# Optimization experiments

Measured on AMD Instinct MI355X. Metric: run time of the kernel, lower is better.

## Reference

```python
import jax, jax.numpy as jnp
import numpy as np

HEADS = 16
D_K = 64  # hidden_size // heads = 1024 // 16
SCALE = D_K ** 0.5


def setup_inputs() -> dict:
    key = jax.random.key(0)
    ks = jax.random.split(key, 7)
    B, S, D = 4, 2048, 1024
    H = 1024  # hidden_size
    O = 1024  # outputs_dims
    s = 0.02
    return {
        "query": jax.random.normal(ks[0], (B, S, D), dtype=jnp.float32),
        "key": jax.random.normal(ks[1], (B, S, D), dtype=jnp.float32),
        "value": jax.random.normal(ks[2], (B, S, D), dtype=jnp.float32),
        "Wq": jax.random.normal(ks[3], (D, H), dtype=jnp.float32) * s,
        "Wk": jax.random.normal(ks[4], (D, H), dtype=jnp.float32) * s,
        "Wv": jax.random.normal(ks[5], (D, H), dtype=jnp.float32) * s,
        "Wo": jax.random.normal(ks[6], (H, O), dtype=jnp.float32) * s,
    }


def reference(query, key, value, Wq, Wk, Wv, Wo):
    B, S, _ = query.shape
    # Dense projections with relu activation (as in the original module)
    q = jax.nn.relu(query @ Wq).reshape(B, S, HEADS, D_K)  # [B,S,H,dk]
    k = jax.nn.relu(key @ Wk).reshape(B, S, HEADS, D_K)
    v = jax.nn.relu(value @ Wv).reshape(B, S, HEADS, D_K)
    # scores: [B,H,Sq,Sk]
    scores = jnp.einsum('bqhd,bkhd->bhqk', q, k) / SCALE
    attn = jax.nn.softmax(scores, axis=-1)
    # attention-weighted values -> [B,Sq,H,dk] -> [B,Sq,H*dk]
    ctx = jnp.einsum('bhqk,bkhd->bqhd', attn, v).reshape(B, S, HEADS * D_K)
    out = jax.nn.relu(ctx @ Wo)
    return out
```

## Files before the change

### kernel.cpp

```cpp
#include <hip/hip_runtime.h>

typedef unsigned short u16;
typedef __bf16 bf16x8 __attribute__((ext_vector_type(8)));
typedef float f32x4 __attribute__((ext_vector_type(4)));
typedef u16 u16x8 __attribute__((ext_vector_type(8)));
typedef u16 u16x4 __attribute__((ext_vector_type(4)));

#define MFMA16(a, b, c) __builtin_amdgcn_mfma_f32_16x16x32_bf16(a, b, c, 0, 0, 0)

static constexpr float QSC = 0.18033688011112042f;

__device__ inline u16 f2bf(float f) {
  union { float f; unsigned u; } x; x.f = f;
  unsigned r = x.u + 0x7FFF + ((x.u >> 16) & 1);
  return (u16)(r >> 16);
}
__device__ inline u16 cvt_bf(float f) {
  __bf16 h = (__bf16)f; return __builtin_bit_cast(u16, h);
}
__device__ inline bf16x8 ld_frag(const u16* p) {
  return __builtin_bit_cast(bf16x8, *(const u16x8*)p);
}
__device__ inline void dma16(const u16* g, u16* l) {
  __builtin_amdgcn_global_load_lds(
      (const __attribute__((address_space(1))) unsigned*)g,
      (__attribute__((address_space(3))) unsigned*)l, 16, 0, 0);
}

#if __has_builtin(__builtin_amdgcn_exp2f)
#define EXP2(x) __builtin_amdgcn_exp2f(x)
#else
#define EXP2(x) exp2f(x)
#endif

__launch_bounds__(256)
__global__ void prep_w(const float* __restrict__ Wq, const float* __restrict__ Wk,
                       const float* __restrict__ Wv, const float* __restrict__ Wo,
                       u16* __restrict__ Wt) {
  __shared__ u16 T[64 * 72];
  const int z = blockIdx.z;
  const float* W = z == 0 ? Wq : z == 1 ? Wk : z == 2 ? Wv : Wo;
  u16* D = Wt + ((size_t)z << 20);
  const int k0 = blockIdx.y * 64, c0 = blockIdx.x * 64;
  const int tid = threadIdx.x;
  const int kr = tid >> 2, cs = (tid & 3) * 16;
  const float* src = W + (size_t)(k0 + kr) * 1024 + c0 + cs;
  float f[16];
#pragma unroll
  for (int i = 0; i < 4; ++i) *(float4*)&f[i * 4] = ((const float4*)src)[i];
#pragma unroll
  for (int i = 0; i < 16; ++i) T[(cs + i) * 72 + kr] = cvt_bf(f[i]);
  __syncthreads();
  const int nn = tid >> 2, ks = (tid & 3) * 16;
  u16* dst = D + (size_t)(c0 + nn) * 1024 + k0 + ks;
  *(u16x8*)dst = *(u16x8*)&T[nn * 72 + ks];
  *(u16x8*)(dst + 8) = *(u16x8*)&T[nn * 72 + ks + 8];
}

__launch_bounds__(256)
__global__ void prep_a(const float* __restrict__ q, const float* __restrict__ k,
                       const float* __restrict__ v, u16* __restrict__ dq,
                       u16* __restrict__ dk, u16* __restrict__ dv) {
  const int z = blockIdx.z;
  const float* s = z == 0 ? q : z == 1 ? k : v;
  u16* d = z == 0 ? dq : z == 1 ? dk : dv;
  for (size_t i = blockIdx.x * 256 + threadIdx.x; i < (size_t)1048576; i += 262144) {
    const float* g = s + i * 8;
    float4 f0 = *(const float4*)g, f1 = *(const float4*)(g + 4);
    u16x8 h;
    h[0] = cvt_bf(f0.x); h[1] = cvt_bf(f0.y); h[2] = cvt_bf(f0.z); h[3] = cvt_bf(f0.w);
    h[4] = cvt_bf(f1.x); h[5] = cvt_bf(f1.y); h[6] = cvt_bf(f1.z); h[7] = cvt_bf(f1.w);
    *(u16x8*)(d + i * 8) = h;
  }
}

__launch_bounds__(512, 2)
__global__ void gemm_fwd(const u16* __restrict__ Aq, const u16* __restrict__ Ak,
                         const u16* __restrict__ Av, const u16* __restrict__ Wt,
                         u16* __restrict__ Qw, u16* __restrict__ Kw,
                         u16* __restrict__ Vw) {
  __shared__ u16 smem[49152];
  const int z = blockIdx.z;
  const u16* A = z == 0 ? Aq : z == 1 ? Ak : Av;
  const u16* Bt = Wt + ((size_t)z << 20);
  u16* out = z == 0 ? Qw : z == 1 ? Kw : Vw;
  const u16* Aop = (z == 2) ? Bt : A;
  const u16* Bop = (z == 2) ? A : Bt;

  const int tid = threadIdx.x;
  const int lane = tid & 63, l15 = lane & 15, quad = lane >> 4;
  const int wv = tid >> 6, wm = wv & 1, wn = wv >> 1;
  const int mblk = ((blockIdx.x & 7) << 2) | (blockIdx.x >> 3);
  const int m0 = (z == 2) ? blockIdx.y * 256 : mblk * 256;
  const int n0 = (z == 2) ? mblk * 256 : blockIdx.y * 256;

  const int cA0 = tid, cA1 = 512 + tid;
  const u16* gA0 = Aop + (size_t)(m0 + (cA0 & 255)) * 1024 + (cA0 >> 8) * 8;
  const u16* gA1 = Aop + (size_t)(m0 + (cA1 & 255)) * 1024 + (cA1 >> 8) * 8;
  const u16* gB0 = Bop + (size_t)(n0 + (cA0 & 255)) * 1024 + (cA0 >> 8) * 8;
  const u16* gB1 = Bop + (size_t)(n0 + (cA1 & 255)) * 1024 + (cA1 >> 8) * 8;
  const int ub0 = (wv * 64) * 8;
  const int ub1 = (512 + wv * 64) * 8;

  const int offA = (quad * 256 + wm * 128 + l15) * 8;
  const int offB = 8192 + (quad * 256 + wn * 64 + l15) * 8;

  f32x4 acc[8][4] = {};

  dma16(gA0, &smem[ub0]);
  dma16(gA1, &smem[ub1]);
  dma16(gB0, &smem[8192 + ub0]);
  dma16(gB1, &smem[8192 + ub1]);
  dma16(gA0 + 32, &smem[16384 + ub0]);
  dma16(gA1 + 32, &smem[16384 + ub1]);
  dma16(gB0 + 32, &smem[16384 + 8192 + ub0]);
  dma16(gB1 + 32, &smem[16384 + 8192 + ub1]);
  asm volatile("s_waitcnt vmcnt(4)" ::: "memory");
  __builtin_amdgcn_sched_barrier(0);
  __builtin_amdgcn_s_barrier();

  int bo0 = 0, bo1 = 16384, bo2 = 32768;
#pragma unroll 1
  for (int t = 0; t < 32; ++t) {
    if (t < 30) {
      dma16(gA0 + (t + 2) * 32, &smem[bo2 + ub0]);
      dma16(gA1 + (t + 2) * 32, &smem[bo2 + ub1]);
    }
    bf16x8 a[4], b[4];
#pragma unroll
    for (int j = 0; j < 4; ++j) b[j] = ld_frag(&smem[bo0 + offB + j * 128]);
#pragma unroll
    for (int i = 0; i < 4; ++i) a[i] = ld_frag(&smem[bo0 + offA + i * 128]);
    asm volatile("s_waitcnt lgkmcnt(0)" ::: "memory");
    __builtin_amdgcn_sched_barrier(0);
    __builtin_amdgcn_s_setprio(1);
#pragma unroll
    for (int i = 0; i < 4; ++i)
#pragma unroll
      for (int j = 0; j < 4; ++j)
        acc[i][j] = MFMA16(a[i], b[j], acc[i][j]);
    __builtin_amdgcn_s_setprio(0);
    __builtin_amdgcn_s_barrier();
    if (t < 30) {
      dma16(gB0 + (t + 2) * 32, &smem[bo2 + 8192 + ub0]);
      dma16(gB1 + (t + 2) * 32, &smem[bo2 + 8192 + ub1]);
    }
#pragma unroll
    for (int i = 0; i < 4; ++i) a[i] = ld_frag(&smem[bo0 + offA + (4 + i) * 128]);
    asm volatile("s_waitcnt lgkmcnt(0)" ::: "memory");
    __builtin_amdgcn_sched_barrier(0);
    __builtin_amdgcn_s_setprio(1);
#pragma unroll
    for (int i = 0; i < 4; ++i)
#pragma unroll
      for (int j = 0; j < 4; ++j)
        acc[4 + i][j] = MFMA16(a[i], b[j], acc[4 + i][j]);
    __builtin_amdgcn_s_setprio(0);
    if (t < 30) {
      asm volatile("s_waitcnt vmcnt(4)" ::: "memory");
      __builtin_amdgcn_sched_barrier(0);
    } else if (t == 30) {
      asm volatile("s_waitcnt vmcnt(0)" ::: "memory");
      __builtin_amdgcn_sched_barrier(0);
    }
    __builtin_amdgcn_s_barrier();
    const int tb = bo0; bo0 = bo1; bo1 = bo2; bo2 = tb;
  }

  if (z < 2) {
    const float sc = z == 0 ? QSC : 1.0f;
#pragma unroll
    for (int i = 0; i < 8; ++i)
#pragma unroll
      for (int j = 0; j < 4; ++j)
#pragma unroll
        for (int r = 0; r < 4; ++r) {
          float v = fmaxf(acc[i][j][r], 0.f) * sc;
          int m = m0 + wm * 128 + i * 16 + quad * 4 + r;
          int n = n0 + wn * 64 + j * 16 + l15;
          out[(size_t)m * 1024 + n] = f2bf(v);
        }
  } else {
    const int bb = n0 >> 11, s0 = n0 & 2047;
#pragma unroll
    for (int half = 0; half < 2; ++half) {
      __syncthreads();
      if ((wn >> 1) == half) {
#pragma unroll
        for (int i = 0; i < 8; ++i)
#pragma unroll
          for (int j = 0; j < 4; ++j)
#pragma unroll
            for (int r = 0; r < 4; ++r) {
              const int row = wm * 128 + i * 16 + quad * 4 + r;
              const int col = (wn & 1) * 64 + j * 16 + l15;
              smem[row * 128 + col] = f2bf(fmaxf(acc[i][j][r], 0.f));
            }
      }
      __syncthreads();
#pragma unroll
      for (int i2 = 0; i2 < 8; ++i2) {
        const int c = i2 * 512 + tid;
        const int row = c >> 4, ch = c & 15;
        u16* dst = out + (size_t)(bb * 1024 + m0 + row) * 2048 + s0 +
                   half * 128 + ch * 8;
        *(u16x8*)dst = *(u16x8*)&smem[row * 128 + ch * 8];
      }
    }
  }
}

__launch_bounds__(256, 3)
__global__ void gemm_out(const u16* __restrict__ A, const u16* __restrict__ Bt,
                         float* __restrict__ out) {
  __shared__ u16 smem[24576];
  const int tid = threadIdx.x;
  const int lane = tid & 63, l15 = lane & 15, quad = lane >> 4;
  const int wv = tid >> 6, wm = wv & 1, wn = wv >> 1;
  const int m0 = (blockIdx.x * 8 + (blockIdx.y >> 3)) * 128;
  const int n0 = (blockIdx.y & 7) * 128;

  const int c0 = tid, c1 = 256 + tid;
  const u16* ga0 = A + (size_t)(m0 + (c0 & 127)) * 1024 + (c0 >> 7) * 8;
  const u16* ga1 = A + (size_t)(m0 + (c1 & 127)) * 1024 + (c1 >> 7) * 8;
  const u16* gb0 = Bt + (size_t)(n0 + (c0 & 127)) * 1024 + (c0 >> 7) * 8;
  const u16* gb1 = Bt + (size_t)(n0 + (c1 & 127)) * 1024 + (c1 >> 7) * 8;
  const int la0 = (wv * 64) * 8, la1 = (256 + wv * 64) * 8;

  f32x4 acc[4][4] = {};

#define STAGE(kt, bo)                                   \
  do {                                                  \
    const int k0_ = (kt) * 32;                          \
    dma16(ga0 + k0_, &smem[(bo) + la0]);                \
    dma16(gb0 + k0_, &smem[(bo) + 4096 + la0]);         \
    dma16(ga1 + k0_, &smem[(bo) + la1]);                \
    dma16(gb1 + k0_, &smem[(bo) + 4096 + la1]);         \
  } while (0)

  STAGE(0, 0);
  STAGE(1, 8192);
  asm volatile("s_waitcnt vmcnt(4)" ::: "memory");
  __builtin_amdgcn_sched_barrier(0);
  __builtin_amdgcn_s_barrier();

  int bo0 = 0, bo1 = 8192, bo2 = 16384;
  const int offA = (quad * 128 + wm * 64 + l15) * 8;
  const int offB = (quad * 128 + wn * 64 + l15) * 8;
#pragma unroll 1
  for (int t = 0; t < 32; ++t) {
    if (t < 30) STAGE(t + 2, bo2);
    const u16* Ab = smem + bo0;
    const u16* Bb = smem + bo0 + 4096;
    bf16x8 a[4], b[4];
#pragma unroll
    for (int i = 0; i < 4; ++i) a[i] = ld_frag(Ab + offA + i * 128);
#pragma unroll
    for (int j = 0; j < 4; ++j) b[j] = ld_frag(Bb + offB + j * 128);
    if (t < 30)
      asm volatile("s_waitcnt vmcnt(4) lgkmcnt(0)" ::: "memory");
    else
      asm volatile("s_waitcnt vmcnt(0) lgkmcnt(0)" ::: "memory");
    __builtin_amdgcn_sched_barrier(0);
    __builtin_amdgcn_s_barrier();
#pragma unroll
    for (int i = 0; i < 4; ++i)
#pragma unroll
      for (int j = 0; j < 4; ++j)
        acc[i][j] = MFMA16(a[i], b[j], acc[i][j]);
    const int tb = bo0; bo0 = bo1; bo1 = bo2; bo2 = tb;
  }
#undef STAGE

#pragma unroll
  for (int i = 0; i < 4; ++i)
#pragma unroll
    for (int j = 0; j < 4; ++j)
#pragma unroll
      for (int r = 0; r < 4; ++r) {
        int m = m0 + wm * 64 + i * 16 + quad * 4 + r;
        int n = n0 + wn * 64 + j * 16 + l15;
        out[(size_t)m * 1024 + n] = fmaxf(acc[i][j][r], 0.f);
      }
}

__launch_bounds__(256, 2)
__global__ void attn(const u16* __restrict__ Q, const u16* __restrict__ K,
                     const u16* __restrict__ V, u16* __restrict__ ctx) {
  __shared__ u16 Ksm[2][4096];
  __shared__ u16 Vsm[2][4096];
  __shared__ u16 Psm[4][4096];

  const int tid = threadIdx.x;
  const int lane = tid & 63, l15 = lane & 15, quad = lane >> 4;
  const int wv = tid >> 6;
  const int bh = blockIdx.x, b = bh >> 4, h = bh & 15;
  const int q0 = blockIdx.y * 256 + wv * 64;

  const u16* Kb = K + ((size_t)b * 2048) * 1024 + h * 64;
  const u16* Vb = V + (size_t)bh * 64 * 2048;
  u16* Pw = Psm[wv];

  const int ck0 = tid, ck1 = 256 + tid;
  const u16* kg0 = Kb + (size_t)(ck0 & 63) * 1024 + (ck0 >> 6) * 8;
  const u16* kg1 = Kb + (size_t)(ck1 & 63) * 1024 + (ck1 >> 6) * 8;
  const u16* vg0 = Vb + (size_t)(ck0 & 63) * 2048 + (ck0 >> 6) * 8;
  const u16* vg1 = Vb + (size_t)(ck1 & 63) * 2048 + (ck1 >> 6) * 8;

  bf16x8 aq[4][2];
#pragma unroll
  for (int qh = 0; qh < 4; ++qh)
#pragma unroll
    for (int kk = 0; kk < 2; ++kk)
      aq[qh][kk] = ld_frag(Q + (size_t)(b * 2048 + q0 + qh * 16 + l15) * 1024 +
                           h * 64 + kk * 32 + quad * 8);

  f32x4 o[4][4] = {};
  float ls[4] = {0.f, 0.f, 0.f, 0.f};

  dma16(kg0, &Ksm[0][ck0 * 8]);
  dma16(kg1, &Ksm[0][ck1 * 8]);
  dma16(vg0, &Vsm[0][ck0 * 8]);
  dma16(vg1, &Vsm[0][ck1 * 8]);

#pragma unroll 1
  for (int t = 0; t < 32; ++t) {
    const int cur = t & 1, nxt = cur ^ 1;
    __syncthreads();

    if (t + 1 < 32) {
      const int kadv = (t + 1) * 64;
      dma16(kg0 + (size_t)kadv * 1024, &Ksm[nxt][ck0 * 8]);
      dma16(kg1 + (size_t)kadv * 1024, &Ksm[nxt][ck1 * 8]);
      dma16(vg0 + kadv, &Vsm[nxt][ck0 * 8]);
      dma16(vg1 + kadv, &Vsm[nxt][ck1 * 8]);
    }

    bf16x8 kf[2][4];
#pragma unroll
    for (int kk = 0; kk < 2; ++kk)
#pragma unroll
      for (int jj = 0; jj < 4; ++jj)
        kf[kk][jj] = ld_frag(&Ksm[cur][((kk * 4 + quad) * 64 + jj * 16 + l15) * 8]);

    f32x4 st[4][4] = {};
    asm volatile("s_waitcnt lgkmcnt(0)" ::: "memory");
    __builtin_amdgcn_sched_barrier(0);
    __builtin_amdgcn_s_setprio(1);
#pragma unroll
    for (int kk = 0; kk < 2; ++kk)
#pragma unroll
      for (int jj = 0; jj < 4; ++jj)
#pragma unroll
        for (int qh = 0; qh < 4; ++qh)
          st[qh][jj] = MFMA16(kf[kk][jj], aq[qh][kk], st[qh][jj]);
    __builtin_amdgcn_s_setprio(0);

#pragma unroll
    for (int qh = 0; qh < 4; ++qh)
#pragma unroll
      for (int jj = 0; jj < 4; ++jj) {
        float p0 = EXP2(st[qh][jj][0]), p1 = EXP2(st[qh][jj][1]);
        float p2 = EXP2(st[qh][jj][2]), p3 = EXP2(st[qh][jj][3]);
        ls[qh] += (p0 + p1) + (p2 + p3);
        u16x4 pk;
        pk[0] = cvt_bf(p0); pk[1] = cvt_bf(p1);
        pk[2] = cvt_bf(p2); pk[3] = cvt_bf(p3);
        const int kc = jj * 2 + (quad >> 1);
        *(u16x4*)&Pw[(kc * 64 + qh * 16 + l15) * 8 + (quad & 1) * 4] = pk;
      }

#pragma unroll
    for (int kk = 0; kk < 2; ++kk) {
      bf16x8 pa[4];
#pragma unroll
      for (int qh = 0; qh < 4; ++qh)
        pa[qh] = ld_frag(&Pw[((kk * 4 + quad) * 64 + qh * 16 + l15) * 8]);
      asm volatile("s_waitcnt lgkmcnt(0)" ::: "memory");
      __builtin_amdgcn_sched_barrier(0);
      __builtin_amdgcn_s_setprio(1);
#pragma unroll
      for (int j = 0; j < 4; ++j) {
        bf16x8 vb = ld_frag(&Vsm[cur][((kk * 4 + quad) * 64 + j * 16 + l15) * 8]);
#pragma unroll
        for (int qh = 0; qh < 4; ++qh)
          o[qh][j] = MFMA16(vb, pa[qh], o[qh][j]);
      }
      __builtin_amdgcn_s_setprio(0);
    }
  }

  float inv[4];
#pragma unroll
  for (int qh = 0; qh < 4; ++qh) {
    ls[qh] += __shfl_xor(ls[qh], 16, 64);
    ls[qh] += __shfl_xor(ls[qh], 32, 64);
    inv[qh] = 1.f / ls[qh];
  }

#pragma unroll
  for (int qh = 0; qh < 4; ++qh) {
    const int tok = b * 2048 + q0 + qh * 16 + l15;
#pragma unroll
    for (int j = 0; j < 4; ++j) {
      u16x4 pk;
#pragma unroll
      for (int r = 0; r < 4; ++r) pk[r] = cvt_bf(o[qh][j][r] * inv[qh]);
      *(u16x4*)&ctx[(size_t)tok * 1024 + h * 64 + j * 16 + quad * 4] = pk;
    }
  }
}

extern "C" void kernel_launch(void* const* d_in, const int* in_sizes, int n_in,
                              void* d_out, int out_size, void* d_ws, size_t ws_size,
                              hipStream_t stream) {
  const float* query = (const float*)d_in[0];
  const float* key   = (const float*)d_in[1];
  const float* value = (const float*)d_in[2];
  const float* Wq = (const float*)d_in[3];
  const float* Wk = (const float*)d_in[4];
  const float* Wv = (const float*)d_in[5];
  const float* Wo = (const float*)d_in[6];
  float* outp = (float*)d_out;

  u16* Wt  = (u16*)d_ws;
  u16* Awq = Wt + ((size_t)4 << 20);
  u16* Qw  = Awq + ((size_t)8 << 20);
  u16* Kw  = Qw + ((size_t)8 << 20);
  u16* Vt  = Kw + ((size_t)8 << 20);
  u16* Awk = (u16*)d_out;
  u16* Awv = Awk + ((size_t)8 << 20);
  u16* Cw  = Awq;

  prep_w<<<dim3(16, 16, 4), 256, 0, stream>>>(Wq, Wk, Wv, Wo, Wt);
  prep_a<<<dim3(1024, 1, 3), 256, 0, stream>>>(query, key, value, Awq, Awk, Awv);
  gemm_fwd<<<dim3(32, 4, 3), 512, 0, stream>>>(Awq, Awk, Awv, Wt, Qw, Kw, Vt);
  attn<<<dim3(64, 8), 256, 0, stream>>>(Qw, Kw, Vt, Cw);
  gemm_out<<<dim3(8, 64), 256, 0, stream>>>(Cw, Wt + ((size_t)3 << 20), outp);
}
```

Measured before the change: 358.7 us.

## Retile projection GEMMs to 256x128 blocks with 4 waves and double buffering

The Q/K/V projection GEMM drops from 512-thread 256x256 tiles with a triple-buffered LDS pipeline to 256-thread 256x128 tiles with double buffering. The V-transpose path gets a new block-id mapping and a single-pass LDS epilogue. The output GEMM moves from 128x128 tiles to the same 256x128 double-buffered scheme with setprio around the MFMAs. The aims are more blocks for better CU fill, less LDS per block and more MFMA work per wave in gemm_out. The cost is a shallower prefetch that waits on vmcnt(0) each step, so memory latency may be less well hidden.

```diff
diff --git a/kernel.cpp b/kernel.cpp
--- a/kernel.cpp
+++ b/kernel.cpp
@@ -74,12 +74,12 @@
   }
 }
 
-__launch_bounds__(512, 2)
+__launch_bounds__(256, 2)
 __global__ void gemm_fwd(const u16* __restrict__ Aq, const u16* __restrict__ Ak,
                          const u16* __restrict__ Av, const u16* __restrict__ Wt,
                          u16* __restrict__ Qw, u16* __restrict__ Kw,
                          u16* __restrict__ Vw) {
-  __shared__ u16 smem[49152];
+  __shared__ u16 smem[32768];
   const int z = blockIdx.z;
   const u16* A = z == 0 ? Aq : z == 1 ? Ak : Av;
   const u16* Bt = Wt + ((size_t)z << 20);
@@ -90,47 +90,52 @@
   const int tid = threadIdx.x;
   const int lane = tid & 63, l15 = lane & 15, quad = lane >> 4;
   const int wv = tid >> 6, wm = wv & 1, wn = wv >> 1;
-  const int mblk = ((blockIdx.x & 7) << 2) | (blockIdx.x >> 3);
-  const int m0 = (z == 2) ? blockIdx.y * 256 : mblk * 256;
-  const int n0 = (z == 2) ? mblk * 256 : blockIdx.y * 256;
-
-  const int cA0 = tid, cA1 = 512 + tid;
-  const u16* gA0 = Aop + (size_t)(m0 + (cA0 & 255)) * 1024 + (cA0 >> 8) * 8;
-  const u16* gA1 = Aop + (size_t)(m0 + (cA1 & 255)) * 1024 + (cA1 >> 8) * 8;
-  const u16* gB0 = Bop + (size_t)(n0 + (cA0 & 255)) * 1024 + (cA0 >> 8) * 8;
-  const u16* gB1 = Bop + (size_t)(n0 + (cA1 & 255)) * 1024 + (cA1 >> 8) * 8;
-  const int ub0 = (wv * 64) * 8;
-  const int ub1 = (512 + wv * 64) * 8;
+  int m0, n0;
+  if (z == 2) {
+    const int id = blockIdx.y * 32 + blockIdx.x;
+    m0 = (id >> 6) * 256;
+    n0 = (id & 63) * 128;
+  } else {
+    const int mblk = ((blockIdx.x & 7) << 2) | (blockIdx.x >> 3);
+    m0 = mblk * 256;
+    n0 = blockIdx.y * 128;
+  }
+
+  const u16* gA[4];
+#pragma unroll
+  for (int i = 0; i < 4; ++i) gA[i] = Aop + (size_t)(m0 + tid) * 1024 + i * 8;
+  const u16* gB[2];
+#pragma unroll
+  for (int i = 0; i < 2; ++i)
+    gB[i] = Bop + (size_t)(n0 + (tid & 127)) * 1024 + (i * 2 + (tid >> 7)) * 8;
 
   const int offA = (quad * 256 + wm * 128 + l15) * 8;
-  const int offB = 8192 + (quad * 256 + wn * 64 + l15) * 8;
+  const int offB = 8192 + (quad * 128 + wn * 64 + l15) * 8;
 
   f32x4 acc[8][4] = {};
 
-  dma16(gA0, &smem[ub0]);
-  dma16(gA1, &smem[ub1]);
-  dma16(gB0, &smem[8192 + ub0]);
-  dma16(gB1, &smem[8192 + ub1]);
-  dma16(gA0 + 32, &smem[16384 + ub0]);
-  dma16(gA1 + 32, &smem[16384 + ub1]);
-  dma16(gB0 + 32, &smem[16384 + 8192 + ub0]);
-  dma16(gB1 + 32, &smem[16384 + 8192 + ub1]);
-  asm volatile("s_waitcnt vmcnt(4)" ::: "memory");
+#pragma unroll
+  for (int i = 0; i < 4; ++i) dma16(gA[i], &smem[i * 2048 + wv * 512]);
+#pragma unroll
+  for (int i = 0; i < 2; ++i) dma16(gB[i], &smem[8192 + i * 2048 + wv * 512]);
+  asm volatile("s_waitcnt vmcnt(0)" ::: "memory");
   __builtin_amdgcn_sched_barrier(0);
   __builtin_amdgcn_s_barrier();
 
-  int bo0 = 0, bo1 = 16384, bo2 = 32768;
 #pragma unroll 1
   for (int t = 0; t < 32; ++t) {
-    if (t < 30) {
-      dma16(gA0 + (t + 2) * 32, &smem[bo2 + ub0]);
-      dma16(gA1 + (t + 2) * 32, &smem[bo2 + ub1]);
+    const int bo = (t & 1) ? 12288 : 0;
+    const int nbo = (t & 1) ? 0 : 12288;
+    if (t + 1 < 32) {
+#pragma unroll
+      for (int i = 0; i < 4; ++i)
+        dma16(gA[i] + (t + 1) * 32, &smem[nbo + i * 2048 + wv * 512]);
     }
     bf16x8 a[4], b[4];
 #pragma unroll
-    for (int j = 0; j < 4; ++j) b[j] = ld_frag(&smem[bo0 + offB + j * 128]);
-#pragma unroll
-    for (int i = 0; i < 4; ++i) a[i] = ld_frag(&smem[bo0 + offA + i * 128]);
+    for (int j = 0; j < 4; ++j) b[j] = ld_frag(&smem[bo + offB + j * 128]);
+#pragma unroll
+    for (int i = 0; i < 4; ++i) a[i] = ld_frag(&smem[bo + offA + i * 128]);
     asm volatile("s_waitcnt lgkmcnt(0)" ::: "memory");
     __builtin_amdgcn_sched_barrier(0);
     __builtin_amdgcn_s_setprio(1);
@@ -141,12 +146,13 @@
         acc[i][j] = MFMA16(a[i], b[j], acc[i][j]);
     __builtin_amdgcn_s_setprio(0);
     __builtin_amdgcn_s_barrier();
-    if (t < 30) {
-      dma16(gB0 + (t + 2) * 32, &smem[bo2 + 8192 + ub0]);
-      dma16(gB1 + (t + 2) * 32, &smem[bo2 + 8192 + ub1]);
-    }
-#pragma unroll
-    for (int i = 0; i < 4; ++i) a[i] = ld_frag(&smem[bo0 + offA + (4 + i) * 128]);
+    if (t + 1 < 32) {
+#pragma unroll
+      for (int i = 0; i < 2; ++i)
+        dma16(gB[i] + (t + 1) * 32, &smem[nbo + 8192 + i * 2048 + wv * 512]);
+    }
+#pragma unroll
+    for (int i = 0; i < 4; ++i) a[i] = ld_frag(&smem[bo + offA + (4 + i) * 128]);
     asm volatile("s_waitcnt lgkmcnt(0)" ::: "memory");
     __builtin_amdgcn_sched_barrier(0);
     __builtin_amdgcn_s_setprio(1);
@@ -156,15 +162,11 @@
       for (int j = 0; j < 4; ++j)
         acc[4 + i][j] = MFMA16(a[i], b[j], acc[4 + i][j]);
     __builtin_amdgcn_s_setprio(0);
-    if (t < 30) {
-      asm volatile("s_waitcnt vmcnt(4)" ::: "memory");
-      __builtin_amdgcn_sched_barrier(0);
-    } else if (t == 30) {
+    if (t + 1 < 32) {
       asm volatile("s_waitcnt vmcnt(0)" ::: "memory");
       __builtin_amdgcn_sched_barrier(0);
     }
     __builtin_amdgcn_s_barrier();
-    const int tb = bo0; bo0 = bo1; bo1 = bo2; bo2 = tb;
   }
 
   if (z < 2) {
@@ -182,103 +184,114 @@
         }
   } else {
     const int bb = n0 >> 11, s0 = n0 & 2047;
-#pragma unroll
-    for (int half = 0; half < 2; ++half) {
-      __syncthreads();
-      if ((wn >> 1) == half) {
-#pragma unroll
-        for (int i = 0; i < 8; ++i)
-#pragma unroll
-          for (int j = 0; j < 4; ++j)
-#pragma unroll
-            for (int r = 0; r < 4; ++r) {
-              const int row = wm * 128 + i * 16 + quad * 4 + r;
-              const int col = (wn & 1) * 64 + j * 16 + l15;
-              smem[row * 128 + col] = f2bf(fmaxf(acc[i][j][r], 0.f));
-            }
-      }
-      __syncthreads();
-#pragma unroll
-      for (int i2 = 0; i2 < 8; ++i2) {
-        const int c = i2 * 512 + tid;
-        const int row = c >> 4, ch = c & 15;
-        u16* dst = out + (size_t)(bb * 1024 + m0 + row) * 2048 + s0 +
-                   half * 128 + ch * 8;
-        *(u16x8*)dst = *(u16x8*)&smem[row * 128 + ch * 8];
-      }
-    }
-  }
-}
-
-__launch_bounds__(256, 3)
+    __syncthreads();
+#pragma unroll
+    for (int i = 0; i < 8; ++i)
+#pragma unroll
+      for (int j = 0; j < 4; ++j)
+#pragma unroll
+        for (int r = 0; r < 4; ++r) {
+          const int row = wm * 128 + i * 16 + quad * 4 + r;
+          const int col = wn * 64 + j * 16 + l15;
+          smem[row * 128 + col] = f2bf(fmaxf(acc[i][j][r], 0.f));
+        }
+    __syncthreads();
+#pragma unroll
+    for (int i2 = 0; i2 < 16; ++i2) {
+      const int c = i2 * 256 + tid;
+      const int row = c >> 4, ch = c & 15;
+      u16* dst = out + (size_t)(bb * 1024 + m0 + row) * 2048 + s0 + ch * 8;
+      *(u16x8*)dst = *(u16x8*)&smem[row * 128 + ch * 8];
+    }
+  }
+}
+
+__launch_bounds__(256, 2)
 __global__ void gemm_out(const u16* __restrict__ A, const u16* __restrict__ Bt,
                          float* __restrict__ out) {
   __shared__ u16 smem[24576];
   const int tid = threadIdx.x;
   const int lane = tid & 63, l15 = lane & 15, quad = lane >> 4;
   const int wv = tid >> 6, wm = wv & 1, wn = wv >> 1;
-  const int m0 = (blockIdx.x * 8 + (blockIdx.y >> 3)) * 128;
-  const int n0 = (blockIdx.y & 7) * 128;
-
-  const int c0 = tid, c1 = 256 + tid;
-  const u16* ga0 = A + (size_t)(m0 + (c0 & 127)) * 1024 + (c0 >> 7) * 8;
-  const u16* ga1 = A + (size_t)(m0 + (c1 & 127)) * 1024 + (c1 >> 7) * 8;
-  const u16* gb0 = Bt + (size_t)(n0 + (c0 & 127)) * 1024 + (c0 >> 7) * 8;
-  const u16* gb1 = Bt + (size_t)(n0 + (c1 & 127)) * 1024 + (c1 >> 7) * 8;
-  const int la0 = (wv * 64) * 8, la1 = (256 + wv * 64) * 8;
-
-  f32x4 acc[4][4] = {};
-
-#define STAGE(kt, bo)                                   \
-  do {                                                  \
-    const int k0_ = (kt) * 32;                          \
-    dma16(ga0 + k0_, &smem[(bo) + la0]);                \
-    dma16(gb0 + k0_, &smem[(bo) + 4096 + la0]);         \
-    dma16(ga1 + k0_, &smem[(bo) + la1]);                \
-    dma16(gb1 + k0_, &smem[(bo) + 4096 + la1]);         \
-  } while (0)
-
-  STAGE(0, 0);
-  STAGE(1, 8192);
-  asm volatile("s_waitcnt vmcnt(4)" ::: "memory");
+  const int mblk = ((blockIdx.x & 7) << 2) | (blockIdx.x >> 3);
+  const int m0 = mblk * 256;
+  const int n0 = blockIdx.y * 128;
+
+  const u16* gA[4];
+#pragma unroll
+  for (int i = 0; i < 4; ++i) gA[i] = A + (size_t)(m0 + tid) * 1024 + i * 8;
+  const u16* gB[2];
+#pragma unroll
+  for (int i = 0; i < 2; ++i)
+    gB[i] = Bt + (size_t)(n0 + (tid & 127)) * 1024 + (i * 2 + (tid >> 7)) * 8;
+
+  const int offA = (quad * 256 + wm * 128 + l15) * 8;
+  const int offB = 8192 + (quad * 128 + wn * 64 + l15) * 8;
+
+  f32x4 acc[8][4] = {};
+
+#pragma unroll
+  for (int i = 0; i < 4; ++i) dma16(gA[i], &smem[i * 2048 + wv * 512]);
+#pragma unroll
+  for (int i = 0; i < 2; ++i) dma16(gB[i], &smem[8192 + i * 2048 + wv * 512]);
+  asm volatile("s_waitcnt vmcnt(0)" ::: "memory");
   __builtin_amdgcn_sched_barrier(0);
   __builtin_amdgcn_s_barrier();
 
-  int bo0 = 0, bo1 = 8192, bo2 = 16384;
-  const int offA = (quad * 128 + wm * 64 + l15) * 8;
-  const int offB = (quad * 128 + wn * 64 + l15) * 8;
 #pragma unroll 1
   for (int t = 0; t < 32; ++t) {
-    if (t < 30) STAGE(t + 2, bo2);
-    const u16* Ab = smem + bo0;
-    const u16* Bb = smem + bo0 + 4096;
+    const int bo = (t & 1) ? 12288 : 0;
+    const int nbo = (t & 1) ? 0 : 12288;
+    if (t + 1 < 32) {
+#pragma unroll
+      for (int i = 0; i < 4; ++i)
+        dma16(gA[i] + (t + 1) * 32, &smem[nbo + i * 2048 + wv * 512]);
+    }
     bf16x8 a[4], b[4];
 #pragma unroll
-    for (int i = 0; i < 4; ++i) a[i] = ld_frag(Ab + offA + i * 128);
-#pragma unroll
-    for (int j = 0; j < 4; ++j) b[j] = ld_frag(Bb + offB + j * 128);
-    if (t < 30)
-      asm volatile("s_waitcnt vmcnt(4) lgkmcnt(0)" ::: "memory");
-    else
-      asm volatile("s_waitcnt vmcnt(0) lgkmcnt(0)" ::: "memory");
+    for (int j = 0; j < 4; ++j) b[j] = ld_frag(&smem[bo + offB + j * 128]);
+#pragma unroll
+    for (int i = 0; i < 4; ++i) a[i] = ld_frag(&smem[bo + offA + i * 128]);
+    asm volatile("s_waitcnt lgkmcnt(0)" ::: "memory");
     __builtin_amdgcn_sched_barrier(0);
+    __builtin_amdgcn_s_setprio(1);
+#pragma unroll
+    for (int i = 0; i < 4; ++i)
+#pragma unroll
+      for (int j = 0; j < 4; ++j)
+        acc[i][j] = MFMA16(a[i], b[j], acc[i][j]);
+    __builtin_amdgcn_s_setprio(0);
     __builtin_amdgcn_s_barrier();
+    if (t + 1 < 32) {
+#pragma unroll
+      for (int i = 0; i < 2; ++i)
+        dma16(gB[i] + (t + 1) * 32, &smem[nbo + 8192 + i * 2048 + wv * 512]);
+    }
+#pragma unroll
+    for (int i = 0; i < 4; ++i) a[i] = ld_frag(&smem[bo + offA + (4 + i) * 128]);
+    asm volatile("s_waitcnt lgkmcnt(0)" ::: "memory");
+    __builtin_amdgcn_sched_barrier(0);
+    __builtin_amdgcn_s_setprio(1);
 #pragma unroll
     for (int i = 0; i < 4; ++i)
 #pragma unroll
       for (int j = 0; j < 4; ++j)
-        acc[i][j] = MFMA16(a[i], b[j], acc[i][j]);
-    const int tb = bo0; bo0 = bo1; bo1 = bo2; bo2 = tb;
-  }
-#undef STAGE
-
-#pragma unroll
-  for (int i = 0; i < 4; ++i)
+        acc[4 + i][j] = MFMA16(a[i], b[j], acc[4 + i][j]);
+    __builtin_amdgcn_s_setprio(0);
+    if (t + 1 < 32) {
+      asm volatile("s_waitcnt vmcnt(0)" ::: "memory");
+      __builtin_amdgcn_sched_barrier(0);
+    }
+    __builtin_amdgcn_s_barrier();
+  }
+
+#pragma unroll
+  for (int i = 0; i < 8; ++i)
 #pragma unroll
     for (int j = 0; j < 4; ++j)
 #pragma unroll
       for (int r = 0; r < 4; ++r) {
-        int m = m0 + wm * 64 + i * 16 + quad * 4 + r;
+        int m = m0 + wm * 128 + i * 16 + quad * 4 + r;
         int n = n0 + wn * 64 + j * 16 + l15;
         out[(size_t)m * 1024 + n] = fmaxf(acc[i][j][r], 0.f);
       }
@@ -434,7 +447,7 @@
 
   prep_w<<<dim3(16, 16, 4), 256, 0, stream>>>(Wq, Wk, Wv, Wo, Wt);
   prep_a<<<dim3(1024, 1, 3), 256, 0, stream>>>(query, key, value, Awq, Awk, Awv);
-  gemm_fwd<<<dim3(32, 4, 3), 512, 0, stream>>>(Awq, Awk, Awv, Wt, Qw, Kw, Vt);
+  gemm_fwd<<<dim3(32, 8, 3), 256, 0, stream>>>(Awq, Awk, Awv, Wt, Qw, Kw, Vt);
   attn<<<dim3(64, 8), 256, 0, stream>>>(Qw, Kw, Vt, Cw);
-  gemm_out<<<dim3(8, 64), 256, 0, stream>>>(Cw, Wt + ((size_t)3 << 20), outp);
-}
+  gemm_out<<<dim3(32, 8), 256, 0, stream>>>(Cw, Wt + ((size_t)3 << 20), outp);
+}
```

New measurement: 368.0 us. 1.03x slower.
